# Performance work log

Measured on AMD Instinct MI355X. Metric: run time of the kernel, lower is better.

Reference implementation:

```python
import jax, jax.numpy as jnp
import numpy as np

B, T, C = 256, 2048, 39   # batch, time, nb_filters
NB = 8                     # number of dilation levels (2**0 .. 2**7)
K = 2                      # kernel size
NC = 8                     # num_classes
EPS = 1e-5                 # BatchNorm eps (eval mode)


def _causal_conv(x, w, b, d):
    """x: [B,C,T], w: [Cout,Cin,K], left-pad (K-1)*d for causality."""
    k = w.shape[-1]
    y = jax.lax.conv_general_dilated(
        x, w, window_strides=(1,), padding=[((k - 1) * d, 0)],
        rhs_dilation=(d,), dimension_numbers=('NCH', 'OIH', 'NCH'))
    return y + b[None, :, None]


def _bn(x, g, be, m, v):
    # eval-mode BatchNorm1d with running stats
    return g[None, :, None] * (x - m[None, :, None]) * jax.lax.rsqrt(v + EPS)[None, :, None] + be[None, :, None]


def _block(x, w, b, g, be, m, v, d):
    # Temporal_Aware_Block, eval mode (dropout = identity).
    # w: [2,C,C,K], b/g/be/m/v: [2,C]
    y = jax.nn.relu(_bn(_causal_conv(x, w[0], b[0], d), g[0], be[0], m[0], v[0]))
    y = jax.nn.relu(_bn(_causal_conv(y, w[1], b[1], d), g[1], be[1], m[1], v[1]))
    # causal conv preserves length, so the 1x1 residual conv branch is never taken
    return x * jax.nn.sigmoid(y)


def setup_inputs() -> dict:
    key = jax.random.key(0)
    ks = jax.random.split(key, 24)
    f = lambda k, s: jax.random.normal(k, s, dtype=jnp.float32) * 0.1
    return {
        'inputs': jax.random.normal(ks[0], (B, T, C), dtype=jnp.float32),
        'conv1x1_w': f(ks[1], (C, C, 1)),
        'conv1x1_b': f(ks[2], (C,)),
        'fw_conv_w': f(ks[3], (NB, 2, C, C, K)),
        'fw_conv_b': f(ks[4], (NB, 2, C)),
        'fw_gamma': 1.0 + f(ks[5], (NB, 2, C)),
        'fw_beta': f(ks[6], (NB, 2, C)),
        'fw_mean': f(ks[7], (NB, 2, C)),
        'fw_var': jax.random.uniform(ks[8], (NB, 2, C), dtype=jnp.float32, minval=0.5, maxval=1.5),
        'bw_conv_w': f(ks[9], (NB, 2, C, C, K)),
        'bw_conv_b': f(ks[10], (NB, 2, C)),
        'bw_gamma': 1.0 + f(ks[11], (NB, 2, C)),
        'bw_beta': f(ks[12], (NB, 2, C)),
        'bw_mean': f(ks[13], (NB, 2, C)),
        'bw_var': jax.random.uniform(ks[14], (NB, 2, C), dtype=jnp.float32, minval=0.5, maxval=1.5),
        'wl_kernel': f(ks[15], (NB, 1)),
        'cls_w': f(ks[16], (NC, C)),
        'cls_b': f(ks[17], (NC,)),
    }


def reference(inputs, conv1x1_w, conv1x1_b,
              fw_conv_w, fw_conv_b, fw_gamma, fw_beta, fw_mean, fw_var,
              bw_conv_w, bw_conv_b, bw_gamma, bw_beta, bw_mean, bw_var,
              wl_kernel, cls_w, cls_b):
    x = jnp.transpose(inputs, (0, 2, 1))           # [B,C,T]
    fwd = _causal_conv(x, conv1x1_w, conv1x1_b, 1)
    bwd = _causal_conv(x[:, :, ::-1], conv1x1_w, conv1x1_b, 1)
    skips = []
    for i in range(NB):
        d = 2 ** i
        fwd = _block(fwd, fw_conv_w[i], fw_conv_b[i], fw_gamma[i], fw_beta[i], fw_mean[i], fw_var[i], d)
        bwd = _block(bwd, bw_conv_w[i], bw_conv_b[i], bw_gamma[i], bw_beta[i], bw_mean[i], bw_var[i], d)
        skips.append(jnp.mean(fwd + bwd, axis=-1))  # [B,C]
    g = jnp.stack(skips, axis=-1)                   # [B,C,NB]
    x2 = jnp.einsum('bcn,no->bc', g, wl_kernel)     # WeightLayer matmul + squeeze
    logits = x2 @ cls_w.T + cls_b                   # [B,NC]
    return jax.nn.log_softmax(logits, axis=1)
```

## Files before the change

### kernel.cpp

```cpp
#include <hip/hip_runtime.h>
#include <math.h>

#define BATCH 256
#define TT    2048
#define CC    39
#define CP    40
#define Y1ST  44
#define NBLK  8
#define KK    2
#define NCLS  8
#define BN_EPS 1e-5f
#define TBLK  512

typedef __attribute__((ext_vector_type(8))) short short8;
typedef __attribute__((ext_vector_type(4))) float floatx4;

__device__ __forceinline__ unsigned short f2b(float f) {
    union { float f; unsigned u; } v; v.f = f;
    unsigned r = v.u + 0x7FFF + ((v.u >> 16) & 1);
    return (unsigned short)(r >> 16);
}
__device__ __forceinline__ unsigned cvtpk(float lo, float hi) {
    unsigned r;
    asm("v_cvt_pk_bf16_f32 %0, %1, %2" : "=v"(r) : "v"(lo), "v"(hi));
    return r;
}
__device__ __forceinline__ float blo(unsigned u) {
    union { unsigned v; float f; } k; k.v = u << 16; return k.f;
}
__device__ __forceinline__ float bhi(unsigned u) {
    union { unsigned v; float f; } k; k.v = u & 0xffff0000u; return k.f;
}
__device__ __forceinline__ void gl_lds16(const void* g, void* l) {
    __builtin_amdgcn_global_load_lds(
        (const __attribute__((address_space(1))) unsigned int*)g,
        (__attribute__((address_space(3))) unsigned int*)l, 16, 0, 0);
}

#define WFB_PER   (2*3*3*512)
#define WFB_TOTAL (2*NBLK*WFB_PER)
#define BFB_TOTAL (2*NBLK*2*48)
#define WFF_TOTAL (3*2*512)
#define BFF_TOTAL 48
#define ZPAD_SHORTS (256 * CP)

__global__ void fold_kernel(const float* __restrict__ fw_w, const float* __restrict__ fw_b,
                            const float* __restrict__ fw_g, const float* __restrict__ fw_be,
                            const float* __restrict__ fw_m, const float* __restrict__ fw_v,
                            const float* __restrict__ bw_w, const float* __restrict__ bw_b,
                            const float* __restrict__ bw_g, const float* __restrict__ bw_be,
                            const float* __restrict__ bw_m, const float* __restrict__ bw_v,
                            const float* __restrict__ c1w, const float* __restrict__ c1b,
                            unsigned short* __restrict__ wfb, float* __restrict__ bfb,
                            unsigned short* __restrict__ wff, float* __restrict__ bff) {
    int idx = blockIdx.x * blockDim.x + threadIdx.x;
    if (idx < WFB_TOTAL) {
        int i = idx;
        int reg = i & 7;   i >>= 3;
        int lane = i & 63; i >>= 6;
        int sl = i % 3;    i /= 3;
        int ct = i % 3;    i /= 3;
        int layer = i & 1; i >>= 1;
        int blk = i & 7;   i >>= 3;
        int dir = i;
        int g = lane >> 4;
        int co = ct * 16 + (lane & 15);
        int p, ci; bool ok = true;
        if (sl < 2) {
            int kin = (g << 3) + reg;
            p = kin >> 4;
            ci = sl * 16 + (kin & 15);
        } else {
            p = g & 1;
            ci = 32 + reg;
            ok = (g < 2);
        }
        float val = 0.f;
        if (ok && co < CC && ci < CC) {
            const float* w = dir ? bw_w : fw_w;
            const float* gam = dir ? bw_g : fw_g;
            const float* var = dir ? bw_v : fw_v;
            int il = blk * 2 + layer;
            float sc = gam[il * CC + co] * rsqrtf(var[il * CC + co] + BN_EPS);
            val = w[((size_t)(il * CC + co) * CC + ci) * KK + p] * sc;
        }
        wfb[idx] = f2b(val);
        return;
    }
    idx -= WFB_TOTAL;
    if (idx < BFB_TOTAL) {
        int co = idx % 48;
        int i = idx / 48;
        int layer = i & 1; i >>= 1;
        int blk = i & 7;   i >>= 3;
        int dir = i;
        float val = 0.f;
        if (co < CC) {
            const float* b  = dir ? bw_b  : fw_b;
            const float* g  = dir ? bw_g  : fw_g;
            const float* be = dir ? bw_be : fw_be;
            const float* m  = dir ? bw_m  : fw_m;
            const float* v  = dir ? bw_v  : fw_v;
            int r = (blk * 2 + layer) * CC + co;
            float sc = g[r] * rsqrtf(v[r] + BN_EPS);
            val = (b[r] - m[r]) * sc + be[r];
        }
        bfb[idx] = val;
        return;
    }
    idx -= BFB_TOTAL;
    if (idx < WFF_TOTAL) {
        int i = idx;
        int reg = i & 7;   i >>= 3;
        int lane = i & 63; i >>= 6;
        int sl = i & 1;    i >>= 1;
        int ct = i;
        int co = ct * 16 + (lane & 15);
        int ci = sl * 32 + ((lane >> 4) << 3) + reg;
        float val = (co < CC && ci < CC) ? c1w[co * CC + ci] : 0.f;
        wff[idx] = f2b(val);
        return;
    }
    idx -= WFF_TOTAL;
    if (idx < BFF_TOTAL) {
        bff[idx] = (idx < CC) ? c1b[idx] : 0.f;
    }
}

__global__ __launch_bounds__(256) void front_mfma(const float* __restrict__ in,
                                                  const unsigned short* __restrict__ wf,
                                                  const float* __restrict__ bias,
                                                  unsigned short* __restrict__ out) {
    __shared__ unsigned short xt[256 * CP + 32];
    const int b = blockIdx.y, t0 = blockIdx.x * 256;
    const int tid = threadIdx.x, lane = tid & 63, wave = tid >> 6;
    const int c = lane & 15, g = lane >> 4;
    const float* src = in + ((size_t)b * TT + t0) * CC;

    unsigned* xd = (unsigned*)xt;
    for (int e = tid; e < 256 * 20; e += 256) {
        int row = e / 20, cp = e - row * 20;
        int c0 = cp * 2;
        float f0 = src[(size_t)row * CC + c0];
        float f1 = (c0 + 1 < CC) ? src[(size_t)row * CC + c0 + 1] : 0.f;
        xd[row * 20 + cp] = cvtpk(f0, f1);
    }
    if (tid < 16) ((unsigned*)(xt + 256 * CP))[tid] = 0;
    __syncthreads();

    short8 Wf[3][2];
#pragma unroll
    for (int ct = 0; ct < 3; ++ct)
#pragma unroll
        for (int sl = 0; sl < 2; ++sl)
            Wf[ct][sl] = *(const short8*)(wf + (((ct * 2 + sl) * 64 + lane) << 3));
    float bs[3][4];
#pragma unroll
    for (int ct = 0; ct < 3; ++ct)
#pragma unroll
        for (int j = 0; j < 4; ++j) bs[ct][j] = bias[ct * 16 + g * 4 + j];

    for (int mt = wave; mt < 16; mt += 4) {
        int row = (mt << 4) + c;
        const unsigned short* bp = xt + row * CP;
        floatx4 acc[3];
#pragma unroll
        for (int ct = 0; ct < 3; ++ct)
            acc[ct] = floatx4{bs[ct][0], bs[ct][1], bs[ct][2], bs[ct][3]};
#pragma unroll
        for (int sl = 0; sl < 2; ++sl) {
            short8 B = *(const short8*)(bp + sl * 32 + g * 8);
#pragma unroll
            for (int ct = 0; ct < 3; ++ct)
                acc[ct] = __builtin_amdgcn_mfma_f32_16x16x32_bf16(Wf[ct][sl], B, acc[ct], 0, 0, 0);
        }
        int t = t0 + row;
        unsigned short* op0 = out + ((size_t)b * TT + t) * CP;
        unsigned short* op1 = out + ((size_t)(BATCH + b) * TT + (TT - 1 - t)) * CP;
#pragma unroll
        for (int ct = 0; ct < 3; ++ct) {
            if (ct == 2 && g >= 2) continue;
            uint2 v;
            v.x = cvtpk(acc[ct][0], acc[ct][1]);
            v.y = cvtpk(acc[ct][2], acc[ct][3]);
            *(uint2*)(op0 + ct * 16 + g * 4) = v;
            *(uint2*)(op1 + ct * 16 + g * 4) = v;
        }
    }
}

template <int D, int TtC>
__global__ __launch_bounds__(TBLK) void block_mfma(const unsigned short* __restrict__ xg,
                                                   unsigned short* __restrict__ yg,
                                                   const unsigned short* __restrict__ wf_all,
                                                   const float* __restrict__ bf_all,
                                                   float* __restrict__ skipPart,
                                                   const unsigned short* __restrict__ zpad,
                                                   int blk, int writeOut) {
    constexpr int NW       = TBLK / 64;
    constexpr int ROWS_X   = TtC + 2 * D;
    constexpr int NCH      = ROWS_X * 5;
    constexpr int NIT      = (NCH + TBLK - 1) / TBLK;
    constexpr int XT_SHORTS = ROWS_X * CP;
    constexpr int M1       = (TtC + D + 15) / 16;
    constexpr int ROWS_Y1  = M1 * 16;
    constexpr int ROWS_REAL = TtC + D;
    constexpr int Y1_SHORTS = ROWS_Y1 * Y1ST + 8;
    constexpr int M2W      = TtC / (16 * NW);

    extern __shared__ char ldsraw[];
    unsigned short* xt = (unsigned short*)ldsraw;
    unsigned short* y1 = xt + XT_SHORTS;
    float* stash = (float*)(y1 + Y1_SHORTS);

    const int dir = blockIdx.z, b = blockIdx.y, tile = blockIdx.x;
    const int t0 = tile * TtC;
    const int tid = threadIdx.x, lane = tid & 63, wave = tid >> 6;
    const int c = lane & 15, g = lane >> 4;

    const size_t cbase = (size_t)(dir * BATCH + b) * TT * CP;
    const unsigned short* wf = wf_all + (size_t)(dir * NBLK + blk) * WFB_PER;
    const float* bf = bf_all + (size_t)(dir * NBLK + blk) * 96;

    {
        const unsigned short* gx = xg + cbase;
#pragma unroll
        for (int it = 0; it < NIT; ++it) {
            int chunk = it * TBLK + wave * 64 + lane;
            if (chunk < NCH) {
                unsigned row = (unsigned)chunk / 5u;
                int sub = chunk - (int)row * 5;
                int t = t0 - 2 * D + (int)row;
                const unsigned short* src = (t >= 0)
                    ? (gx + (size_t)t * CP + sub * 8)
                    : (zpad + (row * CP + sub * 8));
                gl_lds16(src, xt + (size_t)(it * TBLK + wave * 64) * 8);
            }
        }
    }

    short8 Wf[3][3];
#pragma unroll
    for (int ct = 0; ct < 3; ++ct)
#pragma unroll
        for (int sl = 0; sl < 3; ++sl)
            Wf[ct][sl] = *(const short8*)(wf + ((((0 * 3 + ct) * 3 + sl) * 64 + lane) << 3));
    float bs[3][4];
#pragma unroll
    for (int ct = 0; ct < 3; ++ct)
#pragma unroll
        for (int j = 0; j < 4; ++j) bs[ct][j] = bf[ct * 16 + g * 4 + j];

    __syncthreads();

    const int r01off = (g >> 1) * D;
    const int r2off  = (g & 1) * D;
    const int koff8  = (g & 1) << 3;

    for (int mt = wave; mt < M1; mt += NW) {
        int j0 = mt << 4;
        const unsigned short* bp01 = xt + (j0 + c + r01off) * CP + koff8;
        const unsigned short* bp2  = xt + (j0 + c + r2off) * CP + 32;
        short8 B0 = *(const short8*)(bp01);
        short8 B1 = *(const short8*)(bp01 + 16);
        short8 B2 = *(const short8*)(bp2);
        floatx4 acc[3];
#pragma unroll
        for (int ct = 0; ct < 3; ++ct) {
            acc[ct] = floatx4{bs[ct][0], bs[ct][1], bs[ct][2], bs[ct][3]};
            acc[ct] = __builtin_amdgcn_mfma_f32_16x16x32_bf16(Wf[ct][0], B0, acc[ct], 0, 0, 0);
            acc[ct] = __builtin_amdgcn_mfma_f32_16x16x32_bf16(Wf[ct][1], B1, acc[ct], 0, 0, 0);
            acc[ct] = __builtin_amdgcn_mfma_f32_16x16x32_bf16(Wf[ct][2], B2, acc[ct], 0, 0, 0);
        }
        int r = j0 + c;
        bool dead = (t0 - D + r < 0) || (r >= ROWS_REAL);
        unsigned short* yp = y1 + r * Y1ST;
#pragma unroll
        for (int ct = 0; ct < 3; ++ct) {
            if (ct == 2 && g >= 2) continue;
            uint2 v;
            v.x = cvtpk(fmaxf(acc[ct][0], 0.f), fmaxf(acc[ct][1], 0.f));
            v.y = cvtpk(fmaxf(acc[ct][2], 0.f), fmaxf(acc[ct][3], 0.f));
            if (dead) { v.x = 0u; v.y = 0u; }
            *(uint2*)(yp + ct * 16 + g * 4) = v;
        }
    }
    __syncthreads();

#pragma unroll
    for (int ct = 0; ct < 3; ++ct)
#pragma unroll
        for (int sl = 0; sl < 3; ++sl)
            Wf[ct][sl] = *(const short8*)(wf + ((((1 * 3 + ct) * 3 + sl) * 64 + lane) << 3));
#pragma unroll
    for (int ct = 0; ct < 3; ++ct)
#pragma unroll
        for (int j = 0; j < 4; ++j) bs[ct][j] = bf[48 + ct * 16 + g * 4 + j];

    float sums[3][4];
#pragma unroll
    for (int ct = 0; ct < 3; ++ct)
#pragma unroll
        for (int j = 0; j < 4; ++j) sums[ct][j] = 0.f;

#pragma unroll
    for (int mi = 0; mi < M2W; ++mi) {
        int j0 = (wave * M2W + mi) << 4;
        const unsigned short* bp01 = y1 + (j0 + c + r01off) * Y1ST + koff8;
        const unsigned short* bp2  = y1 + (j0 + c + r2off) * Y1ST + 32;
        short8 B0 = *(const short8*)(bp01);
        short8 B1 = *(const short8*)(bp01 + 16);
        short8 B2 = *(const short8*)(bp2);
        floatx4 acc[3];
#pragma unroll
        for (int ct = 0; ct < 3; ++ct) {
            acc[ct] = floatx4{bs[ct][0], bs[ct][1], bs[ct][2], bs[ct][3]};
            acc[ct] = __builtin_amdgcn_mfma_f32_16x16x32_bf16(Wf[ct][0], B0, acc[ct], 0, 0, 0);
            acc[ct] = __builtin_amdgcn_mfma_f32_16x16x32_bf16(Wf[ct][1], B1, acc[ct], 0, 0, 0);
            acc[ct] = __builtin_amdgcn_mfma_f32_16x16x32_bf16(Wf[ct][2], B2, acc[ct], 0, 0, 0);
        }
        int r = j0 + c;
        const unsigned short* xrow = xt + (r + 2 * D) * CP;
        unsigned short* orow = yg + cbase + (size_t)(t0 + r) * CP;
#pragma unroll
        for (int ct = 0; ct < 3; ++ct) {
            uint2 xv = *(const uint2*)(xrow + ct * 16 + g * 4);
            float g0 = blo(xv.x) * __builtin_amdgcn_rcpf(1.f + __expf(-acc[ct][0]));
            float g1 = bhi(xv.x) * __builtin_amdgcn_rcpf(1.f + __expf(-acc[ct][1]));
            float g2 = blo(xv.y) * __builtin_amdgcn_rcpf(1.f + __expf(-acc[ct][2]));
            float g3 = bhi(xv.y) * __builtin_amdgcn_rcpf(1.f + __expf(-acc[ct][3]));
            sums[ct][0] += g0; sums[ct][1] += g1;
            sums[ct][2] += g2; sums[ct][3] += g3;
            if (writeOut && !(ct == 2 && g >= 2)) {
                uint2 v;
                v.x = cvtpk(g0, g1);
                v.y = cvtpk(g2, g3);
                *(uint2*)(orow + ct * 16 + g * 4) = v;
            }
        }
    }
#pragma unroll
    for (int ct = 0; ct < 3; ++ct)
#pragma unroll
        for (int j = 0; j < 4; ++j) {
            float v = sums[ct][j];
            v += __shfl_xor(v, 1, 64);
            v += __shfl_xor(v, 2, 64);
            v += __shfl_xor(v, 4, 64);
            v += __shfl_xor(v, 8, 64);
            sums[ct][j] = v;
        }
    if (c == 0) {
#pragma unroll
        for (int ct = 0; ct < 3; ++ct)
#pragma unroll
            for (int j = 0; j < 4; ++j)
                stash[wave * 48 + ct * 16 + g * 4 + j] = sums[ct][j];
    }
    __syncthreads();
    if (tid < CC) {
        float s = 0.f;
#pragma unroll
        for (int w = 0; w < NW; ++w) s += stash[w * 48 + tid];
        skipPart[(((size_t)(blk * 2 + dir) * BATCH + b) * CC + tid) * 16 + tile] = s;
    }
}

static inline size_t lds_bytes_for(int D, int Tt) {
    int rows_x = Tt + 2 * D;
    int xt_shorts = rows_x * CP;
    int m1 = (Tt + D + 15) / 16;
    int y1_shorts = m1 * 16 * Y1ST + 8;
    return (size_t)(xt_shorts + y1_shorts) * 2 + (TBLK / 64) * 48 * 4;
}

__global__ __launch_bounds__(64) void tail_kernel(const float* __restrict__ skipPart,
                                                  const float* __restrict__ wl,
                                                  const float* __restrict__ cw,
                                                  const float* __restrict__ cb,
                                                  float* __restrict__ out) {
    __shared__ float xs[CC];
    int b = blockIdx.x;
    int cth = threadIdx.x;
    if (cth < CC) {
        float x2 = 0.f;
        for (int i = 0; i < NBLK; ++i) {
            float wli = wl[i] * (1.0f / TT);
            for (int dirn = 0; dirn < 2; ++dirn) {
                const float* sp = skipPart + (((size_t)(i * 2 + dirn) * BATCH + b) * CC + cth) * 16;
                float s = 0.f;
#pragma unroll
                for (int tl = 0; tl < 8; ++tl) s += sp[tl];
                x2 = fmaf(s, wli, x2);
            }
        }
        xs[cth] = x2;
    }
    __syncthreads();
    if (threadIdx.x == 0) {
        float lg[NCLS];
        float mx = -1e30f;
        for (int o = 0; o < NCLS; ++o) {
            float a = cb[o];
#pragma unroll
            for (int cc2 = 0; cc2 < CC; ++cc2) a = fmaf(cw[o * CC + cc2], xs[cc2], a);
            lg[o] = a;
            mx = fmaxf(mx, a);
        }
        float se = 0.f;
        for (int o = 0; o < NCLS; ++o) se += expf(lg[o] - mx);
        float lse = logf(se) + mx;
        for (int o = 0; o < NCLS; ++o) out[b * NCLS + o] = lg[o] - lse;
    }
}

extern "C" void kernel_launch(void* const* d_in, const int* in_sizes, int n_in,
                              void* d_out, int out_size, void* d_ws, size_t ws_size,
                              hipStream_t stream) {
    const float* inputs = (const float*)d_in[0];
    const float* c1w    = (const float*)d_in[1];
    const float* c1b    = (const float*)d_in[2];
    const float* fw_w   = (const float*)d_in[3];
    const float* fw_b   = (const float*)d_in[4];
    const float* fw_g   = (const float*)d_in[5];
    const float* fw_be  = (const float*)d_in[6];
    const float* fw_m   = (const float*)d_in[7];
    const float* fw_v   = (const float*)d_in[8];
    const float* bw_w   = (const float*)d_in[9];
    const float* bw_b   = (const float*)d_in[10];
    const float* bw_g   = (const float*)d_in[11];
    const float* bw_be  = (const float*)d_in[12];
    const float* bw_m   = (const float*)d_in[13];
    const float* bw_v   = (const float*)d_in[14];
    const float* wl     = (const float*)d_in[15];
    const float* clsw   = (const float*)d_in[16];
    const float* clsb   = (const float*)d_in[17];

    const size_t bufsz = (size_t)2 * BATCH * TT * CP;
    unsigned short* buf0 = (unsigned short*)d_ws;
    unsigned short* buf1 = buf0 + bufsz;
    float* skip = (float*)(buf1 + bufsz);
    const size_t skipsz = (size_t)NBLK * 2 * BATCH * CC * 16;
    unsigned short* wfb = (unsigned short*)(skip + skipsz);
    float* bfb = (float*)(wfb + WFB_TOTAL);
    unsigned short* wff = (unsigned short*)(bfb + BFB_TOTAL);
    float* bff = (float*)(wff + WFF_TOTAL);
    unsigned short* zpad = (unsigned short*)(bff + BFF_TOTAL);

    hipMemsetAsync(zpad, 0, ZPAD_SHORTS * sizeof(unsigned short), stream);

    {
        int tot = WFB_TOTAL + BFB_TOTAL + WFF_TOTAL + BFF_TOTAL;
        fold_kernel<<<(tot + 255) / 256, 256, 0, stream>>>(
            fw_w, fw_b, fw_g, fw_be, fw_m, fw_v,
            bw_w, bw_b, bw_g, bw_be, bw_m, bw_v, c1w, c1b,
            wfb, bfb, wff, bff);
    }

    front_mfma<<<dim3(TT / 256, BATCH, 1), 256, 0, stream>>>(inputs, wff, bff, buf0);

    unsigned short* cur = buf0;
    unsigned short* nxt = buf1;
#define LAUNCH_BLOCK(DD)                                                             \
    block_mfma<DD, 256><<<dim3(TT / 256, BATCH, 2), TBLK, lds_bytes_for(DD, 256),    \
                          stream>>>(cur, nxt, wfb, bfb, skip, zpad, i,               \
                                    (i < NBLK - 1) ? 1 : 0)
    for (int i = 0; i < NBLK; ++i) {
        switch (i) {
            case 0: LAUNCH_BLOCK(1); break;
            case 1: LAUNCH_BLOCK(2); break;
            case 2: LAUNCH_BLOCK(4); break;
            case 3: LAUNCH_BLOCK(8); break;
            case 4: LAUNCH_BLOCK(16); break;
            case 5: LAUNCH_BLOCK(32); break;
            case 6: LAUNCH_BLOCK(64); break;
            case 7: LAUNCH_BLOCK(128); break;
        }
        unsigned short* tmp = cur; cur = nxt; nxt = tmp;
    }
#undef LAUNCH_BLOCK

    tail_kernel<<<BATCH, 64, 0, stream>>>(skip, wl, clsw, clsb, (float*)d_out);
}
```

Before: 554.4 us.

## Fuse front 1x1 conv into first dilated temporal block kernel

Replaces the standalone front 1x1 conv kernel with a combined kernel that computes the 1x1 conv for each direction in LDS, with a small causal halo, and then runs dilation-1 block 0 directly. This drops one global write and read of the full bf16 activation tensor for both directions, plus one kernel launch. In exchange the front conv halo rows are recomputed per tile, and the input is read with reversed row indexing for the backward direction.

Result: no change. 558.3 us (+0.7%).

```diff
diff --git a/kernel.cpp b/kernel.cpp
--- a/kernel.cpp
+++ b/kernel.cpp
@@ -11,6 +11,7 @@
 #define NCLS  8
 #define BN_EPS 1e-5f
 #define TBLK  512
+#define NW    8
 
 typedef __attribute__((ext_vector_type(8))) short short8;
 typedef __attribute__((ext_vector_type(4))) float floatx4;
@@ -127,65 +128,209 @@
     }
 }
 
-__global__ __launch_bounds__(256) void front_mfma(const float* __restrict__ in,
-                                                  const unsigned short* __restrict__ wf,
-                                                  const float* __restrict__ bias,
-                                                  unsigned short* __restrict__ out) {
-    __shared__ unsigned short xt[256 * CP + 32];
-    const int b = blockIdx.y, t0 = blockIdx.x * 256;
+__global__ __launch_bounds__(TBLK) void block0_mfma(
+        const float* __restrict__ in,
+        const unsigned short* __restrict__ wf_all, const float* __restrict__ bf_all,
+        const unsigned short* __restrict__ wff, const float* __restrict__ bff,
+        unsigned short* __restrict__ yg, float* __restrict__ skipPart) {
+    constexpr int D = 1;
+    constexpr int ROWS_X   = 272;
+    constexpr int XT_SHORTS = ROWS_X * CP;
+    constexpr int M1       = 17;
+    constexpr int ROWS_REAL = 256 + D;
+    constexpr int Y1_SHORTS = M1 * 16 * Y1ST + 8;
+    constexpr int M2W      = 256 / (16 * NW);
+
+    extern __shared__ char ldsraw[];
+    unsigned short* xt = (unsigned short*)ldsraw;
+    unsigned short* y1 = xt + XT_SHORTS;
+    float* stash = (float*)(y1 + Y1_SHORTS);
+
+    const int dir = blockIdx.z, b = blockIdx.y, tile = blockIdx.x;
+    const int t0 = tile * 256;
     const int tid = threadIdx.x, lane = tid & 63, wave = tid >> 6;
     const int c = lane & 15, g = lane >> 4;
-    const float* src = in + ((size_t)b * TT + t0) * CC;
-
-    unsigned* xd = (unsigned*)xt;
-    for (int e = tid; e < 256 * 20; e += 256) {
-        int row = e / 20, cp = e - row * 20;
-        int c0 = cp * 2;
-        float f0 = src[(size_t)row * CC + c0];
-        float f1 = (c0 + 1 < CC) ? src[(size_t)row * CC + c0 + 1] : 0.f;
-        xd[row * 20 + cp] = cvtpk(f0, f1);
-    }
-    if (tid < 16) ((unsigned*)(xt + 256 * CP))[tid] = 0;
-    __syncthreads();
-
-    short8 Wf[3][2];
-#pragma unroll
-    for (int ct = 0; ct < 3; ++ct)
+    const size_t cbase = (size_t)(dir * BATCH + b) * TT * CP;
+
+    {
+        unsigned* xd = (unsigned*)xt;
+        const float* inb = in + (size_t)b * TT * CC;
+        for (int e = tid; e < ROWS_X * 20; e += TBLK) {
+            int row = e / 20, cp = e - row * 20;
+            int t = t0 - 2 + row;
+            unsigned val = 0u;
+            if (t >= 0 && row < 258) {
+                int srow = dir ? (TT - 1 - t) : t;
+                const float* sp = inb + (size_t)srow * CC + cp * 2;
+                float f0 = sp[0];
+                float f1 = (cp < 19) ? sp[1] : 0.f;
+                val = cvtpk(f0, f1);
+            }
+            xd[e] = val;
+        }
+        if (tid < 16) ((unsigned*)(xt + XT_SHORTS))[tid] = 0;
+    }
+
+    short8 FW[3][2];
+    float fbs[3][4];
+#pragma unroll
+    for (int ct = 0; ct < 3; ++ct) {
 #pragma unroll
         for (int sl = 0; sl < 2; ++sl)
-            Wf[ct][sl] = *(const short8*)(wf + (((ct * 2 + sl) * 64 + lane) << 3));
-    float bs[3][4];
-#pragma unroll
-    for (int ct = 0; ct < 3; ++ct)
-#pragma unroll
-        for (int j = 0; j < 4; ++j) bs[ct][j] = bias[ct * 16 + g * 4 + j];
-
-    for (int mt = wave; mt < 16; mt += 4) {
+            FW[ct][sl] = *(const short8*)(wff + (((ct * 2 + sl) * 64 + lane) << 3));
+#pragma unroll
+        for (int j = 0; j < 4; ++j) fbs[ct][j] = bff[ct * 16 + g * 4 + j];
+    }
+    __syncthreads();
+
+    for (int mt = wave; mt < M1; mt += NW) {
         int row = (mt << 4) + c;
         const unsigned short* bp = xt + row * CP;
         floatx4 acc[3];
 #pragma unroll
         for (int ct = 0; ct < 3; ++ct)
-            acc[ct] = floatx4{bs[ct][0], bs[ct][1], bs[ct][2], bs[ct][3]};
+            acc[ct] = floatx4{fbs[ct][0], fbs[ct][1], fbs[ct][2], fbs[ct][3]};
 #pragma unroll
         for (int sl = 0; sl < 2; ++sl) {
             short8 B = *(const short8*)(bp + sl * 32 + g * 8);
 #pragma unroll
             for (int ct = 0; ct < 3; ++ct)
-                acc[ct] = __builtin_amdgcn_mfma_f32_16x16x32_bf16(Wf[ct][sl], B, acc[ct], 0, 0, 0);
-        }
-        int t = t0 + row;
-        unsigned short* op0 = out + ((size_t)b * TT + t) * CP;
-        unsigned short* op1 = out + ((size_t)(BATCH + b) * TT + (TT - 1 - t)) * CP;
+                acc[ct] = __builtin_amdgcn_mfma_f32_16x16x32_bf16(FW[ct][sl], B, acc[ct], 0, 0, 0);
+        }
+        unsigned short* op = xt + row * CP;
 #pragma unroll
         for (int ct = 0; ct < 3; ++ct) {
             if (ct == 2 && g >= 2) continue;
             uint2 v;
             v.x = cvtpk(acc[ct][0], acc[ct][1]);
             v.y = cvtpk(acc[ct][2], acc[ct][3]);
-            *(uint2*)(op0 + ct * 16 + g * 4) = v;
-            *(uint2*)(op1 + ct * 16 + g * 4) = v;
-        }
+            *(uint2*)(op + ct * 16 + g * 4) = v;
+        }
+    }
+    __syncthreads();
+
+    const int r01off = (g >> 1) * D;
+    const int r2off  = (g & 1) * D;
+    const int koff8  = (g & 1) << 3;
+    const unsigned short* wf = wf_all + (size_t)(dir * NBLK + 0) * WFB_PER;
+    const float* bf = bf_all + (size_t)(dir * NBLK + 0) * 96;
+
+    short8 Wf[3][3];
+    float bs[3][4];
+#pragma unroll
+    for (int ct = 0; ct < 3; ++ct) {
+#pragma unroll
+        for (int sl = 0; sl < 3; ++sl)
+            Wf[ct][sl] = *(const short8*)(wf + (((ct * 3 + sl) * 64 + lane) << 3));
+#pragma unroll
+        for (int j = 0; j < 4; ++j) bs[ct][j] = bf[ct * 16 + g * 4 + j];
+    }
+
+    for (int mt = wave; mt < M1; mt += NW) {
+        int j0 = mt << 4;
+        const unsigned short* bp01 = xt + (j0 + c + r01off) * CP + koff8;
+        const unsigned short* bp2  = xt + (j0 + c + r2off) * CP + 32;
+        short8 B0 = *(const short8*)(bp01);
+        short8 B1 = *(const short8*)(bp01 + 16);
+        short8 B2 = *(const short8*)(bp2);
+        floatx4 acc[3];
+#pragma unroll
+        for (int ct = 0; ct < 3; ++ct) {
+            acc[ct] = floatx4{bs[ct][0], bs[ct][1], bs[ct][2], bs[ct][3]};
+            acc[ct] = __builtin_amdgcn_mfma_f32_16x16x32_bf16(Wf[ct][0], B0, acc[ct], 0, 0, 0);
+            acc[ct] = __builtin_amdgcn_mfma_f32_16x16x32_bf16(Wf[ct][1], B1, acc[ct], 0, 0, 0);
+            acc[ct] = __builtin_amdgcn_mfma_f32_16x16x32_bf16(Wf[ct][2], B2, acc[ct], 0, 0, 0);
+        }
+        int r = j0 + c;
+        bool dead = (t0 - D + r < 0) || (r >= ROWS_REAL);
+        unsigned short* yp = y1 + r * Y1ST;
+#pragma unroll
+        for (int ct = 0; ct < 3; ++ct) {
+            if (ct == 2 && g >= 2) continue;
+            uint2 v;
+            v.x = cvtpk(fmaxf(acc[ct][0], 0.f), fmaxf(acc[ct][1], 0.f));
+            v.y = cvtpk(fmaxf(acc[ct][2], 0.f), fmaxf(acc[ct][3], 0.f));
+            if (dead) { v.x = 0u; v.y = 0u; }
+            *(uint2*)(yp + ct * 16 + g * 4) = v;
+        }
+    }
+    __syncthreads();
+
+#pragma unroll
+    for (int ct = 0; ct < 3; ++ct) {
+#pragma unroll
+        for (int sl = 0; sl < 3; ++sl)
+            Wf[ct][sl] = *(const short8*)(wf + ((((3 + ct) * 3 + sl) * 64 + lane) << 3));
+#pragma unroll
+        for (int j = 0; j < 4; ++j) bs[ct][j] = bf[48 + ct * 16 + g * 4 + j];
+    }
+
+    float sums[3][4];
+#pragma unroll
+    for (int ct = 0; ct < 3; ++ct)
+#pragma unroll
+        for (int j = 0; j < 4; ++j) sums[ct][j] = 0.f;
+
+#pragma unroll
+    for (int mi = 0; mi < M2W; ++mi) {
+        int j0 = (((wave * M2W) + mi) << 4);
+        const unsigned short* bp01 = y1 + (j0 + c + r01off) * Y1ST + koff8;
+        const unsigned short* bp2  = y1 + (j0 + c + r2off) * Y1ST + 32;
+        short8 B0 = *(const short8*)(bp01);
+        short8 B1 = *(const short8*)(bp01 + 16);
+        short8 B2 = *(const short8*)(bp2);
+        floatx4 acc[3];
+#pragma unroll
+        for (int ct = 0; ct < 3; ++ct) {
+            acc[ct] = floatx4{bs[ct][0], bs[ct][1], bs[ct][2], bs[ct][3]};
+            acc[ct] = __builtin_amdgcn_mfma_f32_16x16x32_bf16(Wf[ct][0], B0, acc[ct], 0, 0, 0);
+            acc[ct] = __builtin_amdgcn_mfma_f32_16x16x32_bf16(Wf[ct][1], B1, acc[ct], 0, 0, 0);
+            acc[ct] = __builtin_amdgcn_mfma_f32_16x16x32_bf16(Wf[ct][2], B2, acc[ct], 0, 0, 0);
+        }
+        int r = j0 + c;
+        const unsigned short* xrow = xt + (r + 2 * D) * CP;
+        unsigned short* orow = yg + cbase + (size_t)(t0 + r) * CP;
+#pragma unroll
+        for (int ct = 0; ct < 3; ++ct) {
+            uint2 xv = *(const uint2*)(xrow + ct * 16 + g * 4);
+            float g0 = blo(xv.x) * __builtin_amdgcn_rcpf(1.f + __expf(-acc[ct][0]));
+            float g1 = bhi(xv.x) * __builtin_amdgcn_rcpf(1.f + __expf(-acc[ct][1]));
+            float g2 = blo(xv.y) * __builtin_amdgcn_rcpf(1.f + __expf(-acc[ct][2]));
+            float g3 = bhi(xv.y) * __builtin_amdgcn_rcpf(1.f + __expf(-acc[ct][3]));
+            sums[ct][0] += g0; sums[ct][1] += g1;
+            sums[ct][2] += g2; sums[ct][3] += g3;
+            if (!(ct == 2 && g >= 2)) {
+                uint2 v;
+                v.x = cvtpk(g0, g1);
+                v.y = cvtpk(g2, g3);
+                *(uint2*)(orow + ct * 16 + g * 4) = v;
+            }
+        }
+    }
+#pragma unroll
+    for (int ct = 0; ct < 3; ++ct)
+#pragma unroll
+        for (int j = 0; j < 4; ++j) {
+            float v = sums[ct][j];
+            v += __shfl_xor(v, 1, 64);
+            v += __shfl_xor(v, 2, 64);
+            v += __shfl_xor(v, 4, 64);
+            v += __shfl_xor(v, 8, 64);
+            sums[ct][j] = v;
+        }
+    if (c == 0) {
+#pragma unroll
+        for (int ct = 0; ct < 3; ++ct)
+#pragma unroll
+            for (int j = 0; j < 4; ++j)
+                stash[wave * 48 + ct * 16 + g * 4 + j] = sums[ct][j];
+    }
+    __syncthreads();
+    if (tid < CC) {
+        float s = 0.f;
+#pragma unroll
+        for (int w = 0; w < NW; ++w) s += stash[w * 48 + tid];
+        skipPart[(((size_t)(0 * 2 + dir) * BATCH + b) * CC + tid) * 16 + tile] = s;
     }
 }
 
@@ -197,16 +342,15 @@
                                                    float* __restrict__ skipPart,
                                                    const unsigned short* __restrict__ zpad,
                                                    int blk, int writeOut) {
-    constexpr int NW       = TBLK / 64;
+    constexpr int NW_      = TBLK / 64;
     constexpr int ROWS_X   = TtC + 2 * D;
     constexpr int NCH      = ROWS_X * 5;
     constexpr int NIT      = (NCH + TBLK - 1) / TBLK;
     constexpr int XT_SHORTS = ROWS_X * CP;
     constexpr int M1       = (TtC + D + 15) / 16;
-    constexpr int ROWS_Y1  = M1 * 16;
     constexpr int ROWS_REAL = TtC + D;
-    constexpr int Y1_SHORTS = ROWS_Y1 * Y1ST + 8;
-    constexpr int M2W      = TtC / (16 * NW);
+    constexpr int Y1_SHORTS = M1 * 16 * Y1ST + 8;
+    constexpr int M2W      = TtC / (16 * NW_);
 
     extern __shared__ char ldsraw[];
     unsigned short* xt = (unsigned short*)ldsraw;
@@ -257,7 +401,7 @@
     const int r2off  = (g & 1) * D;
     const int koff8  = (g & 1) << 3;
 
-    for (int mt = wave; mt < M1; mt += NW) {
+    for (int mt = wave; mt < M1; mt += NW_) {
         int j0 = mt << 4;
         const unsigned short* bp01 = xt + (j0 + c + r01off) * CP + koff8;
         const unsigned short* bp2  = xt + (j0 + c + r2off) * CP + 32;
@@ -361,7 +505,7 @@
     if (tid < CC) {
         float s = 0.f;
 #pragma unroll
-        for (int w = 0; w < NW; ++w) s += stash[w * 48 + tid];
+        for (int w = 0; w < NW_; ++w) s += stash[w * 48 + tid];
         skipPart[(((size_t)(blk * 2 + dir) * BATCH + b) * CC + tid) * 16 + tile] = s;
     }
 }
@@ -457,7 +601,11 @@
             wfb, bfb, wff, bff);
     }
 
-    front_mfma<<<dim3(TT / 256, BATCH, 1), 256, 0, stream>>>(inputs, wff, bff, buf0);
+    {
+        size_t lds0 = (size_t)(272 * CP + 17 * 16 * Y1ST + 8) * 2 + (TBLK / 64) * 48 * 4 + 64;
+        block0_mfma<<<dim3(TT / 256, BATCH, 2), TBLK, lds0, stream>>>(
+            inputs, wfb, bfb, wff, bff, buf0, skip);
+    }
 
     unsigned short* cur = buf0;
     unsigned short* nxt = buf1;
@@ -465,9 +613,8 @@
     block_mfma<DD, 256><<<dim3(TT / 256, BATCH, 2), TBLK, lds_bytes_for(DD, 256),    \
                           stream>>>(cur, nxt, wfb, bfb, skip, zpad, i,               \
                                     (i < NBLK - 1) ? 1 : 0)
-    for (int i = 0; i < NBLK; ++i) {
+    for (int i = 1; i < NBLK; ++i) {
         switch (i) {
-            case 0: LAUNCH_BLOCK(1); break;
             case 1: LAUNCH_BLOCK(2); break;
             case 2: LAUNCH_BLOCK(4); break;
             case 3: LAUNCH_BLOCK(8); break;
```
